# Kernel tuning notes

Measured on AMD Instinct MI355X. Metric: run time of the kernel, lower is better.

## Reference

```python
import jax, jax.numpy as jnp
import numpy as np

NUM_HEADS = 16
ENCODE_DIM = 1024
KEY_DIM = 64
VALUE_DIM = 64
B, T = 2, 2048
NEG_INF = -1e30  # large negative instead of -inf for grad safety; same softmax result


def setup_inputs() -> dict:
    key = jax.random.key(0)
    ks = jax.random.split(key, 8)
    s_in = 1.0 / np.sqrt(ENCODE_DIM)
    s_out = 1.0 / np.sqrt(NUM_HEADS * VALUE_DIM)
    return {
        "K": jax.random.normal(ks[0], (B, T, ENCODE_DIM), jnp.float32),
        "Q": jax.random.normal(ks[1], (B, T, ENCODE_DIM), jnp.float32),
        "V": jax.random.normal(ks[2], (B, T, ENCODE_DIM), jnp.float32),
        # per-head projection weights stacked along head axis: [H, C, d]
        "Wk": jax.random.normal(ks[3], (NUM_HEADS, ENCODE_DIM, KEY_DIM), jnp.float32) * s_in,
        "Wq": jax.random.normal(ks[4], (NUM_HEADS, ENCODE_DIM, KEY_DIM), jnp.float32) * s_in,
        "Wv": jax.random.normal(ks[5], (NUM_HEADS, ENCODE_DIM, VALUE_DIM), jnp.float32) * s_in,
        # output projection: concat over heads -> encode_dim, with bias
        "Wo": jax.random.normal(ks[6], (NUM_HEADS * VALUE_DIM, ENCODE_DIM), jnp.float32) * s_out,
        "bo": jax.random.normal(ks[7], (ENCODE_DIM,), jnp.float32) * 0.01,
    }


def reference(K, Q, V, Wk, Wq, Wv, Wo, bo):
    # Batched per-head projections (original loops over heads with separate Linears)
    k = jnp.einsum('btc,hcd->bhtd', K, Wk)  # [B,H,T,dk]
    q = jnp.einsum('btc,hcd->bhtd', Q, Wq)  # [B,H,T,dk]
    v = jnp.einsum('btc,hcd->bhtd', V, Wv)  # [B,H,T,dv]
    scores = jnp.einsum('bhtd,bhsd->bhts', q, k)  # [B,H,T,T]
    t = scores.shape[-1]
    causal = jnp.tril(jnp.ones((t, t), bool))
    scores = jnp.where(causal, scores, NEG_INF)
    # original: mask first, then scale by 1/sqrt(key_dim), then softmax
    attn = jax.nn.softmax(scores * (1.0 / (KEY_DIM ** 0.5)), axis=-1)
    # dropout is identity in eval mode
    out = jnp.einsum('bhts,bhsd->bhtd', attn, v)  # [B,H,T,dv]
    b, h, tt, dv = out.shape
    concat = out.transpose(0, 2, 1, 3).reshape(b, tt, h * dv)  # head concat order matches loop
    return concat @ Wo + bo
```

## Files before the change

kernel.cpp:

```cpp
#include <hip/hip_runtime.h>
#include <hip/hip_bf16.h>

typedef __bf16 bf16_t;
typedef __bf16 bf16x4 __attribute__((ext_vector_type(4)));
typedef __bf16 bf16x8 __attribute__((ext_vector_type(8)));
typedef float f32x4 __attribute__((ext_vector_type(4)));
typedef unsigned int u32;

static __device__ __forceinline__ u32 pk2(float a, float b) {
    union { u32 u; bf16_t h[2]; } w;
    w.h[0] = (bf16_t)a; w.h[1] = (bf16_t)b;
    return w.u;
}

#define GLOAD_LDS16(gsrc, ldst)                                                  \
    __builtin_amdgcn_global_load_lds(                                            \
        (const __attribute__((address_space(1))) void*)(gsrc),                   \
        (__attribute__((address_space(3))) void*)(ldst), 16, 0, 0)

__global__ void conv_whead_t(const float* __restrict__ in, bf16_t* __restrict__ out) {
    __shared__ bf16_t t[64][72];
    const int tc = blockIdx.x, h = blockIdx.y;
    const int tid = threadIdx.x;
#pragma unroll
    for (int p = 0; p < 4; ++p) {
        int r = p * 16 + (tid >> 4);
        int c4 = (tid & 15) * 4;
        float4 x = *(const float4*)(in + (size_t)h * 65536 + (size_t)(tc * 64 + r) * 64 + c4);
        t[r][c4 + 0] = (bf16_t)x.x; t[r][c4 + 1] = (bf16_t)x.y;
        t[r][c4 + 2] = (bf16_t)x.z; t[r][c4 + 3] = (bf16_t)x.w;
    }
    __syncthreads();
#pragma unroll
    for (int p = 0; p < 2; ++p) {
        int d = p * 32 + (tid >> 3);
        int c8 = (tid & 7) * 8;
        bf16x8 v;
#pragma unroll
        for (int j = 0; j < 8; ++j) v[j] = t[c8 + j][d];
        *(bf16x8*)(out + (size_t)(h * 64 + d) * 1024 + tc * 64 + c8) = v;
    }
}

__global__ void conv_wo_t(const float* __restrict__ in, bf16_t* __restrict__ out) {
    __shared__ bf16_t t[64][72];
    const int r0 = blockIdx.x * 64;
    const int c0 = blockIdx.y * 64;
    const int tid = threadIdx.x;
#pragma unroll
    for (int p = 0; p < 4; ++p) {
        int r = p * 16 + (tid >> 4);
        int c4 = (tid & 15) * 4;
        float4 x = *(const float4*)(in + (size_t)(r0 + r) * 1024 + c0 + c4);
        t[r][c4 + 0] = (bf16_t)x.x; t[r][c4 + 1] = (bf16_t)x.y;
        t[r][c4 + 2] = (bf16_t)x.z; t[r][c4 + 3] = (bf16_t)x.w;
    }
    __syncthreads();
#pragma unroll
    for (int p = 0; p < 2; ++p) {
        int d = p * 32 + (tid >> 3);
        int c8 = (tid & 7) * 8;
        bf16x8 v;
#pragma unroll
        for (int j = 0; j < 8; ++j) v[j] = t[c8 + j][d];
        *(bf16x8*)(out + (size_t)(c0 + d) * 1024 + r0 + c8) = v;
    }
}

template<int BM, bool A_F32, bool OUT_F32, bool BIAS>
__device__ __forceinline__
void gemm_core(const void* Ap, const bf16_t* Bt, void* Cp, const float* bias,
               int m0, int n0) {
    constexpr int N = 1024, K = 1024, BK = 32;
    constexpr int APAD = A_F32 ? 8 : 0;
    constexpr int MI = BM / 32;
    __shared__ bf16_t As[2][BM][BK + APAD];
    __shared__ bf16_t Bs[2][128][BK];

    const int tid = threadIdx.x;
    const int wv = tid >> 6, l = tid & 63;
    const int ln16 = l & 15, g8 = (l >> 4) * 8;
    const int wr = (wv >> 1) * (BM / 2), wc = (wv & 1) * 64;
    const int srow = l >> 2, scol = (l & 3) * 8;

    const float*  Af = (const float*)Ap;
    const bf16_t* Ab = (const bf16_t*)Ap;

    f32x4 zero = {0.f, 0.f, 0.f, 0.f};
    f32x4 acc[MI][4];
#pragma unroll
    for (int i = 0; i < MI; ++i)
#pragma unroll
        for (int j = 0; j < 4; ++j) acc[i][j] = zero;

    auto stage = [&](int buf, int k0) {
#pragma unroll
        for (int i = 0; i < BM / 64; ++i) {
            int row = wv * (BM / 4) + i * 16;
            if constexpr (A_F32) {
                const float* s = Af + (size_t)(m0 + row + srow) * K + k0 + scol;
                float4 x0 = *(const float4*)s;
                float4 x1 = *(const float4*)(s + 4);
                bf16x8 v;
                v[0] = (bf16_t)x0.x; v[1] = (bf16_t)x0.y; v[2] = (bf16_t)x0.z; v[3] = (bf16_t)x0.w;
                v[4] = (bf16_t)x1.x; v[5] = (bf16_t)x1.y; v[6] = (bf16_t)x1.z; v[7] = (bf16_t)x1.w;
                *(bf16x8*)&As[buf][row + srow][scol] = v;
            } else {
                GLOAD_LDS16(Ab + (size_t)(m0 + row + srow) * K + k0 + scol,
                            &As[buf][row][0]);
            }
        }
#pragma unroll
        for (int i = 0; i < 2; ++i) {
            int row = wv * 32 + i * 16;
            GLOAD_LDS16(Bt + (size_t)(n0 + row + srow) * K + k0 + scol,
                        &Bs[buf][row][0]);
        }
    };

    stage(0, 0);
    __syncthreads();
    for (int kt = 0; kt < K / BK; ++kt) {
        int cur = kt & 1;
        if (kt + 1 < K / BK) stage(cur ^ 1, (kt + 1) * BK);
        bf16x8 a[MI], b[4];
#pragma unroll
        for (int i = 0; i < MI; ++i)
            a[i] = *(const bf16x8*)&As[cur][wr + i * 16 + ln16][g8];
#pragma unroll
        for (int i = 0; i < 4; ++i)
            b[i] = *(const bf16x8*)&Bs[cur][wc + i * 16 + ln16][g8];
#pragma unroll
        for (int mi = 0; mi < MI; ++mi)
#pragma unroll
            for (int ni = 0; ni < 4; ++ni)
                acc[mi][ni] = __builtin_amdgcn_mfma_f32_16x16x32_bf16(
                    a[mi], b[ni], acc[mi][ni], 0, 0, 0);
        __syncthreads();
    }

    float*  Cf = (float*)Cp;
    bf16_t* Cb = (bf16_t*)Cp;
#pragma unroll
    for (int mi = 0; mi < MI; ++mi)
#pragma unroll
        for (int ni = 0; ni < 4; ++ni)
#pragma unroll
            for (int r = 0; r < 4; ++r) {
                int row = m0 + wr + mi * 16 + (l >> 4) * 4 + r;
                int col = n0 + wc + ni * 16 + ln16;
                float v = acc[mi][ni][r];
                if constexpr (BIAS) v += bias[col];
                if constexpr (OUT_F32) Cf[(size_t)row * N + col] = v;
                else                   Cb[(size_t)row * N + col] = (bf16_t)v;
            }
}

__global__ __launch_bounds__(256, 3)
void gemm_proj(const float* A0, const float* A1, const float* A2,
               const bf16_t* B0, const bf16_t* B1, const bf16_t* B2,
               bf16_t* C0, bf16_t* C1, bf16_t* C2) {
    int z = blockIdx.z;
    const float* A = (z == 0) ? A0 : (z == 1) ? A1 : A2;
    const bf16_t* B = (z == 0) ? B0 : (z == 1) ? B1 : B2;
    bf16_t* C = (z == 0) ? C0 : (z == 1) ? C1 : C2;
    gemm_core<128, true, false, false>(A, B, C, nullptr, blockIdx.x * 128, blockIdx.y * 128);
}

__global__ __launch_bounds__(256, 2)
void gemm_out(const bf16_t* A, const bf16_t* Bt, void* C, const float* bias) {
    gemm_core<64, false, true, true>(A, Bt, C, bias, blockIdx.x * 64, blockIdx.y * 128);
}

__global__ void transpose_bf16(const bf16_t* __restrict__ in, bf16_t* __restrict__ out) {
    __shared__ bf16_t t[64][72];
    const int b = blockIdx.z;
    const int r0 = blockIdx.x * 64;
    const int c0 = blockIdx.y * 64;
    const bf16_t* src = in + (size_t)b * 2048 * 1024;
    bf16_t* dst = out + (size_t)b * 1024 * 2048;
    const int tid = threadIdx.x;
    const int row = tid >> 3, c8 = (tid & 7) * 8;
#pragma unroll
    for (int i = 0; i < 2; ++i)
        *(int4*)&t[row + i * 32][c8] =
            *(const int4*)(src + (size_t)(r0 + row + i * 32) * 1024 + c0 + c8);
    __syncthreads();
#pragma unroll
    for (int i = 0; i < 2; ++i) {
        int orow = row + i * 32;
        bf16x8 v;
#pragma unroll
        for (int j = 0; j < 8; ++j) v[j] = t[c8 + j][orow];
        *(bf16x8*)(dst + (size_t)(c0 + orow) * 2048 + r0 + c8) = v;
    }
}

__global__ __launch_bounds__(256, 2)
void attn_causal(const bf16_t* __restrict__ qp, const bf16_t* __restrict__ kp,
                 const bf16_t* __restrict__ vtp, bf16_t* __restrict__ op) {
    constexpr int T = 2048, HC = 1024;
    constexpr float SC2 = 0.18033688011112042f;
    constexpr float THR = 7.0f;
    __shared__ u32 Pex[4][32][32];

    const int tid = threadIdx.x;
    const int wid = tid >> 6, ln = tid & 63;
    const int q16 = ln & 15, g = ln >> 4, g8 = g * 8;
    const u32 swz = (u32)(q16 & 7) << 2;

    const int c = blockIdx.x;
    const int bh = c & 31;
    const int j = (c >> 5) & 7;
    const int half = (c >> 8) & 1;
    const int gidx = j * 4 + wid;
    const int strip = half ? (63 - gidx) : gidx;
    const int qbase = strip * 32;
    const int ntiles = strip / 2 + 1;

    const int b = bh >> 4, h = bh & 15;
    const bf16_t* Q  = qp  + (size_t)b * T * HC + (size_t)h * 64;
    const bf16_t* Kg = kp  + (size_t)b * T * HC + (size_t)h * 64;
    const bf16_t* Vt = vtp + (size_t)b * HC * T + (size_t)h * 64 * T;

    int qrow[2];
    bf16x8 qf[2][2];
#pragma unroll
    for (int st = 0; st < 2; ++st) {
        qrow[st] = qbase + st * 16 + q16;
        qf[st][0] = *(const bf16x8*)(Q + (size_t)qrow[st] * HC + g8);
        qf[st][1] = *(const bf16x8*)(Q + (size_t)qrow[st] * HC + 32 + g8);
    }

    float m[2] = {-3.0e38f, -3.0e38f}, l[2] = {0.f, 0.f};
    f32x4 zero = {0.f, 0.f, 0.f, 0.f};
    f32x4 oacc[2][4];
#pragma unroll
    for (int st = 0; st < 2; ++st)
#pragma unroll
        for (int i = 0; i < 4; ++i) oacc[st][i] = zero;

    bf16x8 ka[4][2];
    bf16x8 va[2][4];
#pragma unroll
    for (int sb = 0; sb < 4; ++sb) {
        const bf16_t* kr = Kg + (size_t)(sb * 16 + q16) * HC;
        ka[sb][0] = *(const bf16x8*)(kr + g8);
        ka[sb][1] = *(const bf16x8*)(kr + 32 + g8);
    }
#pragma unroll
    for (int kc = 0; kc < 2; ++kc)
#pragma unroll
        for (int nf = 0; nf < 4; ++nf)
            va[kc][nf] = *(const bf16x8*)(Vt + (size_t)(nf * 16 + q16) * T
                                          + kc * 32 + g8);

    for (int t = 0; t < ntiles; ++t) {
        const int kv0 = t * 64;
        const bool last = (t == ntiles - 1);
        const int kvn = (t + 1 < ntiles ? t + 1 : ntiles - 1) * 64;

        float zs[2][4][4];
        __builtin_amdgcn_s_setprio(1);
#pragma unroll
        for (int sb = 0; sb < 4; ++sb) {
            int sbase = kv0 + sb * 16 + 4 * g;
#pragma unroll
            for (int st = 0; st < 2; ++st) {
                f32x4 z = zero;
                z = __builtin_amdgcn_mfma_f32_16x16x32_bf16(ka[sb][0], qf[st][0], z, 0, 0, 0);
                z = __builtin_amdgcn_mfma_f32_16x16x32_bf16(ka[sb][1], qf[st][1], z, 0, 0, 0);
                if (last) {
#pragma unroll
                    for (int r = 0; r < 4; ++r)
                        zs[st][sb][r] = (sbase + r <= qrow[st]) ? z[r] * SC2 : -1.0e30f;
                } else {
#pragma unroll
                    for (int r = 0; r < 4; ++r) zs[st][sb][r] = z[r] * SC2;
                }
            }
        }
        __builtin_amdgcn_s_setprio(0);

#pragma unroll
        for (int sb = 0; sb < 4; ++sb) {
            const bf16_t* kr = Kg + (size_t)(kvn + sb * 16 + q16) * HC;
            ka[sb][0] = *(const bf16x8*)(kr + g8);
            ka[sb][1] = *(const bf16x8*)(kr + 32 + g8);
        }

        float pm[2];
#pragma unroll
        for (int st = 0; st < 2; ++st) {
            float a0 = zs[st][0][0];
#pragma unroll
            for (int sb = 0; sb < 4; ++sb)
#pragma unroll
                for (int r = 0; r < 4; ++r) a0 = fmaxf(a0, zs[st][sb][r]);
            a0 = fmaxf(a0, __shfl_xor(a0, 16, 64));
            a0 = fmaxf(a0, __shfl_xor(a0, 32, 64));
            pm[st] = a0;
        }
        bool defer = (pm[0] <= m[0] + THR) && (pm[1] <= m[1] + THR);
        if (!__all((int)defer)) {
#pragma unroll
            for (int st = 0; st < 2; ++st) {
                float newm = fmaxf(m[st], pm[st]);
                float alpha = exp2f(m[st] - newm);
                m[st] = newm;
                l[st] *= alpha;
                float ar[4];
#pragma unroll
                for (int r = 0; r < 4; ++r) ar[r] = __shfl(alpha, 4 * g + r, 64);
#pragma unroll
                for (int nf = 0; nf < 4; ++nf)
#pragma unroll
                    for (int r = 0; r < 4; ++r) oacc[st][nf][r] *= ar[r];
            }
        }

#pragma unroll
        for (int st = 0; st < 2; ++st) {
            f32x4 ps4 = zero;
#pragma unroll
            for (int sb = 0; sb < 4; ++sb) {
                float e0 = exp2f(zs[st][sb][0] - m[st]);
                float e1 = exp2f(zs[st][sb][1] - m[st]);
                float e2 = exp2f(zs[st][sb][2] - m[st]);
                float e3 = exp2f(zs[st][sb][3] - m[st]);
                ps4[0] += e0; ps4[1] += e1; ps4[2] += e2; ps4[3] += e3;
                uint2 w;
                w.x = pk2(e0, e1);
                w.y = pk2(e2, e3);
                u32 colA = ((u32)(sb * 8 + 2 * g)) ^ swz;
                *(uint2*)&Pex[wid][st * 16 + q16][colA] = w;
            }
            float psum = ps4[0] + ps4[1] + ps4[2] + ps4[3];
            psum += __shfl_xor(psum, 16, 64);
            psum += __shfl_xor(psum, 32, 64);
            l[st] += psum;
        }

        __builtin_amdgcn_s_setprio(1);
#pragma unroll
        for (int kc = 0; kc < 2; ++kc) {
            bf16x8 pa[2];
#pragma unroll
            for (int st = 0; st < 2; ++st) {
                u32 colR = ((u32)(kc * 16 + 4 * g)) ^ swz;
                pa[st] = *(const bf16x8*)&Pex[wid][st * 16 + q16][colR];
            }
#pragma unroll
            for (int nf = 0; nf < 4; ++nf)
#pragma unroll
                for (int st = 0; st < 2; ++st)
                    oacc[st][nf] = __builtin_amdgcn_mfma_f32_16x16x32_bf16(
                        pa[st], va[kc][nf], oacc[st][nf], 0, 0, 0);
        }
        __builtin_amdgcn_s_setprio(0);

#pragma unroll
        for (int kc = 0; kc < 2; ++kc)
#pragma unroll
            for (int nf = 0; nf < 4; ++nf)
                va[kc][nf] = *(const bf16x8*)(Vt + (size_t)(nf * 16 + q16) * T
                                              + kvn + kc * 32 + g8);
    }

    bf16_t* O = op + (size_t)b * T * HC + (size_t)h * 64;
#pragma unroll
    for (int st = 0; st < 2; ++st) {
        int base = qbase + st * 16;
#pragma unroll
        for (int r = 0; r < 4; ++r) {
            float lr = __shfl(l[st], 4 * g + r, 64);
            float inv = 1.0f / lr;
#pragma unroll
            for (int nf = 0; nf < 4; ++nf)
                O[(size_t)(base + 4 * g + r) * HC + nf * 16 + q16] =
                    (bf16_t)(oacc[st][nf][r] * inv);
        }
    }
}


extern "C" void kernel_launch(void* const* d_in, const int* in_sizes, int n_in,
                              void* d_out, int out_size, void* d_ws, size_t ws_size,
                              hipStream_t stream) {
    const float* K_in = (const float*)d_in[0];
    const float* Q_in = (const float*)d_in[1];
    const float* V_in = (const float*)d_in[2];
    const float* Wk   = (const float*)d_in[3];
    const float* Wq   = (const float*)d_in[4];
    const float* Wv   = (const float*)d_in[5];
    const float* Wo   = (const float*)d_in[6];
    const float* bo   = (const float*)d_in[7];

    char* ws = (char*)d_ws;
    const size_t MB = 1024 * 1024;
    bf16_t* Wqt = (bf16_t*)(ws + 0 * MB);
    bf16_t* Wkt = (bf16_t*)(ws + 2 * MB);
    bf16_t* Wvt = (bf16_t*)(ws + 4 * MB);
    bf16_t* Wot = (bf16_t*)(ws + 6 * MB);
    bf16_t* qp  = (bf16_t*)(ws + 8 * MB);
    bf16_t* kp  = (bf16_t*)(ws + 16 * MB);
    bf16_t* vp  = (bf16_t*)(ws + 24 * MB);
    bf16_t* vt  = (bf16_t*)(ws + 32 * MB);
    bf16_t* ao  = (bf16_t*)(ws + 24 * MB);

    conv_whead_t<<<dim3(16, 16), 256, 0, stream>>>(Wq, Wqt);
    conv_whead_t<<<dim3(16, 16), 256, 0, stream>>>(Wk, Wkt);
    conv_whead_t<<<dim3(16, 16), 256, 0, stream>>>(Wv, Wvt);
    conv_wo_t<<<dim3(16, 16), 256, 0, stream>>>(Wo, Wot);

    gemm_proj<<<dim3(32, 8, 3), 256, 0, stream>>>(Q_in, K_in, V_in,
                                                  Wqt, Wkt, Wvt,
                                                  qp, kp, vp);

    transpose_bf16<<<dim3(32, 16, 2), 256, 0, stream>>>(vp, vt);

    attn_causal<<<512, 256, 0, stream>>>(qp, kp, vt, ao);

    gemm_out<<<dim3(64, 8), 256, 0, stream>>>(ao, Wot, d_out, bo);
}
```

Baseline: 150.0 us.

## Split each causal query strip's KV range across two warps and merge via LDS

```diff
diff --git a/kernel.cpp b/kernel.cpp
--- a/kernel.cpp
+++ b/kernel.cpp
@@ -203,6 +203,8 @@
     constexpr float SC2 = 0.18033688011112042f;
     constexpr float THR = 7.0f;
     __shared__ u32 Pex[4][32][32];
+    __shared__ float MLbuf[4][64][4];
+    __shared__ float Obuf[2][64][32];
 
     const int tid = threadIdx.x;
     const int wid = tid >> 6, ln = tid & 63;
@@ -211,175 +213,220 @@
 
     const int c = blockIdx.x;
     const int bh = c & 31;
-    const int j = (c >> 5) & 7;
-    const int half = (c >> 8) & 1;
-    const int gidx = j * 4 + wid;
-    const int strip = half ? (63 - gidx) : gidx;
-    const int qbase = strip * 32;
-    const int ntiles = strip / 2 + 1;
+    const int p = (c >> 5) & 15;
+    const int hw = wid >> 1;
+    const int half = wid & 1;
 
     const int b = bh >> 4, h = bh & 15;
     const bf16_t* Q  = qp  + (size_t)b * T * HC + (size_t)h * 64;
     const bf16_t* Kg = kp  + (size_t)b * T * HC + (size_t)h * 64;
     const bf16_t* Vt = vtp + (size_t)b * HC * T + (size_t)h * 64 * T;
-
-    int qrow[2];
-    bf16x8 qf[2][2];
-#pragma unroll
-    for (int st = 0; st < 2; ++st) {
-        qrow[st] = qbase + st * 16 + q16;
-        qf[st][0] = *(const bf16x8*)(Q + (size_t)qrow[st] * HC + g8);
-        qf[st][1] = *(const bf16x8*)(Q + (size_t)qrow[st] * HC + 32 + g8);
-    }
-
-    float m[2] = {-3.0e38f, -3.0e38f}, l[2] = {0.f, 0.f};
+    bf16_t* O = op + (size_t)b * T * HC + (size_t)h * 64;
+
     f32x4 zero = {0.f, 0.f, 0.f, 0.f};
-    f32x4 oacc[2][4];
-#pragma unroll
-    for (int st = 0; st < 2; ++st)
-#pragma unroll
-        for (int i = 0; i < 4; ++i) oacc[st][i] = zero;
-
-    bf16x8 ka[4][2];
-    bf16x8 va[2][4];
-#pragma unroll
-    for (int sb = 0; sb < 4; ++sb) {
-        const bf16_t* kr = Kg + (size_t)(sb * 16 + q16) * HC;
-        ka[sb][0] = *(const bf16x8*)(kr + g8);
-        ka[sb][1] = *(const bf16x8*)(kr + 32 + g8);
-    }
-#pragma unroll
-    for (int kc = 0; kc < 2; ++kc)
-#pragma unroll
-        for (int nf = 0; nf < 4; ++nf)
-            va[kc][nf] = *(const bf16x8*)(Vt + (size_t)(nf * 16 + q16) * T
-                                          + kc * 32 + g8);
-
-    for (int t = 0; t < ntiles; ++t) {
-        const int kv0 = t * 64;
-        const bool last = (t == ntiles - 1);
-        const int kvn = (t + 1 < ntiles ? t + 1 : ntiles - 1) * 64;
-
-        float zs[2][4][4];
-        __builtin_amdgcn_s_setprio(1);
+
+#pragma unroll
+    for (int slot = 0; slot < 2; ++slot) {
+        const int strip = (slot == 0) ? (2 * p + hw) : (63 - 2 * p - hw);
+        const int qbase = strip * 32;
+        const int len  = strip / 2 + 1;
+        const int hcut = (len + 1) >> 1;
+        const int t0 = half ? hcut : 0;
+        const int t1 = half ? len : hcut;
+
+        int qrow[2];
+        bf16x8 qf[2][2];
+#pragma unroll
+        for (int st = 0; st < 2; ++st) {
+            qrow[st] = qbase + st * 16 + q16;
+            qf[st][0] = *(const bf16x8*)(Q + (size_t)qrow[st] * HC + g8);
+            qf[st][1] = *(const bf16x8*)(Q + (size_t)qrow[st] * HC + 32 + g8);
+        }
+
+        float m[2] = {-3.0e38f, -3.0e38f}, l[2] = {0.f, 0.f};
+        f32x4 oacc[2][4];
+#pragma unroll
+        for (int st = 0; st < 2; ++st)
+#pragma unroll
+            for (int i = 0; i < 4; ++i) oacc[st][i] = zero;
+
+        bf16x8 ka[4][2], va[2][4];
 #pragma unroll
         for (int sb = 0; sb < 4; ++sb) {
-            int sbase = kv0 + sb * 16 + 4 * g;
-#pragma unroll
-            for (int st = 0; st < 2; ++st) {
-                f32x4 z = zero;
-                z = __builtin_amdgcn_mfma_f32_16x16x32_bf16(ka[sb][0], qf[st][0], z, 0, 0, 0);
-                z = __builtin_amdgcn_mfma_f32_16x16x32_bf16(ka[sb][1], qf[st][1], z, 0, 0, 0);
-                if (last) {
-#pragma unroll
-                    for (int r = 0; r < 4; ++r)
-                        zs[st][sb][r] = (sbase + r <= qrow[st]) ? z[r] * SC2 : -1.0e30f;
-                } else {
-#pragma unroll
-                    for (int r = 0; r < 4; ++r) zs[st][sb][r] = z[r] * SC2;
-                }
-            }
-        }
-        __builtin_amdgcn_s_setprio(0);
-
-#pragma unroll
-        for (int sb = 0; sb < 4; ++sb) {
-            const bf16_t* kr = Kg + (size_t)(kvn + sb * 16 + q16) * HC;
+            const bf16_t* kr = Kg + (size_t)(t0 * 64 + sb * 16 + q16) * HC;
             ka[sb][0] = *(const bf16x8*)(kr + g8);
             ka[sb][1] = *(const bf16x8*)(kr + 32 + g8);
         }
-
-        float pm[2];
-#pragma unroll
-        for (int st = 0; st < 2; ++st) {
-            float a0 = zs[st][0][0];
-#pragma unroll
-            for (int sb = 0; sb < 4; ++sb)
-#pragma unroll
-                for (int r = 0; r < 4; ++r) a0 = fmaxf(a0, zs[st][sb][r]);
-            a0 = fmaxf(a0, __shfl_xor(a0, 16, 64));
-            a0 = fmaxf(a0, __shfl_xor(a0, 32, 64));
-            pm[st] = a0;
-        }
-        bool defer = (pm[0] <= m[0] + THR) && (pm[1] <= m[1] + THR);
-        if (!__all((int)defer)) {
-#pragma unroll
-            for (int st = 0; st < 2; ++st) {
-                float newm = fmaxf(m[st], pm[st]);
-                float alpha = exp2f(m[st] - newm);
-                m[st] = newm;
-                l[st] *= alpha;
-                float ar[4];
-#pragma unroll
-                for (int r = 0; r < 4; ++r) ar[r] = __shfl(alpha, 4 * g + r, 64);
-#pragma unroll
-                for (int nf = 0; nf < 4; ++nf)
-#pragma unroll
-                    for (int r = 0; r < 4; ++r) oacc[st][nf][r] *= ar[r];
-            }
-        }
-
-#pragma unroll
-        for (int st = 0; st < 2; ++st) {
-            f32x4 ps4 = zero;
-#pragma unroll
-            for (int sb = 0; sb < 4; ++sb) {
-                float e0 = exp2f(zs[st][sb][0] - m[st]);
-                float e1 = exp2f(zs[st][sb][1] - m[st]);
-                float e2 = exp2f(zs[st][sb][2] - m[st]);
-                float e3 = exp2f(zs[st][sb][3] - m[st]);
-                ps4[0] += e0; ps4[1] += e1; ps4[2] += e2; ps4[3] += e3;
-                uint2 w;
-                w.x = pk2(e0, e1);
-                w.y = pk2(e2, e3);
-                u32 colA = ((u32)(sb * 8 + 2 * g)) ^ swz;
-                *(uint2*)&Pex[wid][st * 16 + q16][colA] = w;
-            }
-            float psum = ps4[0] + ps4[1] + ps4[2] + ps4[3];
-            psum += __shfl_xor(psum, 16, 64);
-            psum += __shfl_xor(psum, 32, 64);
-            l[st] += psum;
-        }
-
-        __builtin_amdgcn_s_setprio(1);
-#pragma unroll
-        for (int kc = 0; kc < 2; ++kc) {
-            bf16x8 pa[2];
-#pragma unroll
-            for (int st = 0; st < 2; ++st) {
-                u32 colR = ((u32)(kc * 16 + 4 * g)) ^ swz;
-                pa[st] = *(const bf16x8*)&Pex[wid][st * 16 + q16][colR];
-            }
-#pragma unroll
-            for (int nf = 0; nf < 4; ++nf)
-#pragma unroll
-                for (int st = 0; st < 2; ++st)
-                    oacc[st][nf] = __builtin_amdgcn_mfma_f32_16x16x32_bf16(
-                        pa[st], va[kc][nf], oacc[st][nf], 0, 0, 0);
-        }
-        __builtin_amdgcn_s_setprio(0);
-
 #pragma unroll
         for (int kc = 0; kc < 2; ++kc)
 #pragma unroll
             for (int nf = 0; nf < 4; ++nf)
                 va[kc][nf] = *(const bf16x8*)(Vt + (size_t)(nf * 16 + q16) * T
-                                              + kvn + kc * 32 + g8);
-    }
-
-    bf16_t* O = op + (size_t)b * T * HC + (size_t)h * 64;
-#pragma unroll
-    for (int st = 0; st < 2; ++st) {
-        int base = qbase + st * 16;
-#pragma unroll
-        for (int r = 0; r < 4; ++r) {
-            float lr = __shfl(l[st], 4 * g + r, 64);
-            float inv = 1.0f / lr;
-#pragma unroll
-            for (int nf = 0; nf < 4; ++nf)
-                O[(size_t)(base + 4 * g + r) * HC + nf * 16 + q16] =
-                    (bf16_t)(oacc[st][nf][r] * inv);
-        }
+                                              + t0 * 64 + kc * 32 + g8);
+
+        for (int gt = t0; gt < t1; ++gt) {
+            const int kv0 = gt * 64;
+            const bool last = (gt == len - 1);
+            const int kvn = ((gt + 1 < t1) ? gt + 1 : gt) * 64;
+
+            float zs[2][4][4];
+            __builtin_amdgcn_s_setprio(1);
+#pragma unroll
+            for (int sb = 0; sb < 4; ++sb) {
+                int sbase = kv0 + sb * 16 + 4 * g;
+#pragma unroll
+                for (int st = 0; st < 2; ++st) {
+                    f32x4 z = zero;
+                    z = __builtin_amdgcn_mfma_f32_16x16x32_bf16(ka[sb][0], qf[st][0], z, 0, 0, 0);
+                    z = __builtin_amdgcn_mfma_f32_16x16x32_bf16(ka[sb][1], qf[st][1], z, 0, 0, 0);
+                    if (last) {
+#pragma unroll
+                        for (int r = 0; r < 4; ++r)
+                            zs[st][sb][r] = (sbase + r <= qrow[st]) ? z[r] * SC2 : -1.0e30f;
+                    } else {
+#pragma unroll
+                        for (int r = 0; r < 4; ++r) zs[st][sb][r] = z[r] * SC2;
+                    }
+                }
+            }
+            __builtin_amdgcn_s_setprio(0);
+
+#pragma unroll
+            for (int sb = 0; sb < 4; ++sb) {
+                const bf16_t* kr = Kg + (size_t)(kvn + sb * 16 + q16) * HC;
+                ka[sb][0] = *(const bf16x8*)(kr + g8);
+                ka[sb][1] = *(const bf16x8*)(kr + 32 + g8);
+            }
+
+            float pm[2];
+#pragma unroll
+            for (int st = 0; st < 2; ++st) {
+                float a0 = zs[st][0][0];
+#pragma unroll
+                for (int sb = 0; sb < 4; ++sb)
+#pragma unroll
+                    for (int r = 0; r < 4; ++r) a0 = fmaxf(a0, zs[st][sb][r]);
+                a0 = fmaxf(a0, __shfl_xor(a0, 16, 64));
+                a0 = fmaxf(a0, __shfl_xor(a0, 32, 64));
+                pm[st] = a0;
+            }
+            bool defer = (pm[0] <= m[0] + THR) && (pm[1] <= m[1] + THR);
+            if (!__all((int)defer)) {
+#pragma unroll
+                for (int st = 0; st < 2; ++st) {
+                    float newm = fmaxf(m[st], pm[st]);
+                    float alpha = exp2f(m[st] - newm);
+                    m[st] = newm;
+                    l[st] *= alpha;
+                    float ar[4];
+#pragma unroll
+                    for (int r = 0; r < 4; ++r) ar[r] = __shfl(alpha, 4 * g + r, 64);
+#pragma unroll
+                    for (int nf = 0; nf < 4; ++nf)
+#pragma unroll
+                        for (int r = 0; r < 4; ++r) oacc[st][nf][r] *= ar[r];
+                }
+            }
+
+#pragma unroll
+            for (int st = 0; st < 2; ++st) {
+                f32x4 ps4 = zero;
+#pragma unroll
+                for (int sb = 0; sb < 4; ++sb) {
+                    float e0 = exp2f(zs[st][sb][0] - m[st]);
+                    float e1 = exp2f(zs[st][sb][1] - m[st]);
+                    float e2 = exp2f(zs[st][sb][2] - m[st]);
+                    float e3 = exp2f(zs[st][sb][3] - m[st]);
+                    ps4[0] += e0; ps4[1] += e1; ps4[2] += e2; ps4[3] += e3;
+                    uint2 w;
+                    w.x = pk2(e0, e1);
+                    w.y = pk2(e2, e3);
+                    u32 colA = ((u32)(sb * 8 + 2 * g)) ^ swz;
+                    *(uint2*)&Pex[wid][st * 16 + q16][colA] = w;
+                }
+                float psum = ps4[0] + ps4[1] + ps4[2] + ps4[3];
+                psum += __shfl_xor(psum, 16, 64);
+                psum += __shfl_xor(psum, 32, 64);
+                l[st] += psum;
+            }
+
+            __builtin_amdgcn_s_setprio(1);
+#pragma unroll
+            for (int kc = 0; kc < 2; ++kc) {
+                bf16x8 pa[2];
+#pragma unroll
+                for (int st = 0; st < 2; ++st) {
+                    u32 colR = ((u32)(kc * 16 + 4 * g)) ^ swz;
+                    pa[st] = *(const bf16x8*)&Pex[wid][st * 16 + q16][colR];
+                }
+#pragma unroll
+                for (int nf = 0; nf < 4; ++nf)
+#pragma unroll
+                    for (int st = 0; st < 2; ++st)
+                        oacc[st][nf] = __builtin_amdgcn_mfma_f32_16x16x32_bf16(
+                            pa[st], va[kc][nf], oacc[st][nf], 0, 0, 0);
+            }
+            __builtin_amdgcn_s_setprio(0);
+
+#pragma unroll
+            for (int kc = 0; kc < 2; ++kc)
+#pragma unroll
+                for (int nf = 0; nf < 4; ++nf)
+                    va[kc][nf] = *(const bf16x8*)(Vt + (size_t)(nf * 16 + q16) * T
+                                                  + kvn + kc * 32 + g8);
+        }
+
+        MLbuf[wid][ln][0] = m[0];
+        MLbuf[wid][ln][1] = m[1];
+        MLbuf[wid][ln][2] = l[0];
+        MLbuf[wid][ln][3] = l[1];
+        __syncthreads();
+        const int pw = wid ^ 1;
+        float ms[2], sa[2], lm[2];
+#pragma unroll
+        for (int st = 0; st < 2; ++st) {
+            float mB = MLbuf[pw][ln][st];
+            float lB = MLbuf[pw][ln][2 + st];
+            ms[st] = fmaxf(m[st], mB);
+            sa[st] = exp2f(m[st] - ms[st]);
+            lm[st] = l[st] * sa[st] + lB * exp2f(mB - ms[st]);
+        }
+        if (half) {
+#pragma unroll
+            for (int st = 0; st < 2; ++st) {
+                float ar[4];
+#pragma unroll
+                for (int r = 0; r < 4; ++r) ar[r] = __shfl(sa[st], 4 * g + r, 64);
+#pragma unroll
+                for (int nf = 0; nf < 4; ++nf)
+#pragma unroll
+                    for (int r = 0; r < 4; ++r)
+                        Obuf[hw][ln][st * 16 + nf * 4 + r] = oacc[st][nf][r] * ar[r];
+            }
+        }
+        __syncthreads();
+        if (!half) {
+#pragma unroll
+            for (int st = 0; st < 2; ++st) {
+                float ar[4], lr[4];
+#pragma unroll
+                for (int r = 0; r < 4; ++r) {
+                    ar[r] = __shfl(sa[st], 4 * g + r, 64);
+                    lr[r] = __shfl(lm[st], 4 * g + r, 64);
+                }
+#pragma unroll
+                for (int r = 0; r < 4; ++r) {
+                    float inv = 1.0f / lr[r];
+#pragma unroll
+                    for (int nf = 0; nf < 4; ++nf) {
+                        float v = oacc[st][nf][r] * ar[r] + Obuf[hw][ln][st * 16 + nf * 4 + r];
+                        O[(size_t)(qbase + st * 16 + 4 * g + r) * HC + nf * 16 + q16] =
+                            (bf16_t)(v * inv);
+                    }
+                }
+            }
+        }
+        __syncthreads();
     }
 }
 
```

Result: slower. 154.4 us (+2.9%).
